# Performance work log

Hardware: AMD Instinct MI355X
Metric: run time of the kernel (lower is better)

Reference implementation:

```python
import jax, jax.numpy as jnp
import numpy as np

B, T, D, H = 2, 2048, 1024, 16
HS = D // H  # head_size = 64


def setup_inputs() -> dict:
    key = jax.random.key(0)
    ks = jax.random.split(key, 8)
    scale = D ** -0.5
    q = jax.random.normal(ks[0], (B, T, D), dtype=jnp.float32)
    k = jax.random.normal(ks[1], (B, T, D), dtype=jnp.float32)
    v = jax.random.normal(ks[2], (B, T, D), dtype=jnp.float32)
    # per-head projection weights (no bias), stacked over heads: [H, D, HS]
    Wq = jax.random.normal(ks[3], (H, D, HS), dtype=jnp.float32) * scale
    Wk = jax.random.normal(ks[4], (H, D, HS), dtype=jnp.float32) * scale
    Wv = jax.random.normal(ks[5], (H, D, HS), dtype=jnp.float32) * scale
    # output projection Linear(H*HS, D) with bias
    Wo = jax.random.normal(ks[6], (D, D), dtype=jnp.float32) * scale
    bo = jnp.zeros((D,), dtype=jnp.float32)
    # causal mask, broadcastable to [B, T, T]; mask==0 -> -inf
    mask = jnp.tril(jnp.ones((T, T), dtype=bool))[None]
    return {"q": q, "k": k, "v": v, "Wq": Wq, "Wk": Wk, "Wv": Wv,
            "Wo": Wo, "bo": bo, "mask": mask}


def reference(q, k, v, Wq, Wk, Wv, Wo, bo, mask):
    # Batched equivalent of the per-head loop: project all heads at once.
    Q = jnp.einsum('btc,hcd->bhtd', q, Wq)  # [B,H,T,HS]
    K = jnp.einsum('btc,hcd->bhtd', k, Wk)
    V = jnp.einsum('btc,hcd->bhtd', v, Wv)
    wei = jnp.einsum('bhtd,bhsd->bhts', Q, K) * (HS ** -0.5)  # [B,H,T,T]
    wei = jnp.where(mask[:, None, :, :], wei, jnp.float32(-jnp.inf))
    attn = jax.nn.softmax(wei, axis=-1)  # dropout is identity in eval
    out = jnp.einsum('bhts,bhsd->bhtd', attn, V)
    out = out.transpose(0, 2, 1, 3).reshape(B, T, D)  # concat heads
    return out @ Wo + bo
```

## Files before the change

### kernel.cpp

```cpp
#include <hip/hip_runtime.h>
#include <hip/hip_bf16.h>
#include <math.h>

#define BB 2
#define TT 2048
#define DM 1024
#define NH 16
#define HS 64
#define MM (BB*TT)

typedef __attribute__((ext_vector_type(8))) short s16x8;
typedef __attribute__((ext_vector_type(4))) float f32x4;

#define MFMA16(a,b,c) __builtin_amdgcn_mfma_f32_16x16x32_bf16((a),(b),(c),0,0,0)

__device__ inline unsigned short f2bf(float f) {
    union { float f; unsigned u; } x; x.f = f;
    unsigned r = x.u + 0x7fff + ((x.u >> 16) & 1);
    return (unsigned short)(r >> 16);
}
__device__ inline unsigned short f2bfr(float f) {
    union { float f; unsigned u; } x; x.f = f;
    return (unsigned short)((x.u + 0x8000u) >> 16);
}

__device__ __forceinline__ void gload16(const void* g, void* l) {
    __builtin_amdgcn_global_load_lds(
        (const __attribute__((address_space(1))) unsigned int*)g,
        (__attribute__((address_space(3))) unsigned int*)l, 16, 0, 0);
}

__global__ __launch_bounds__(256) void cvt_w_kernel(
    const float* __restrict__ W0, const float* __restrict__ W1,
    const float* __restrict__ W2, unsigned short* __restrict__ dst, int wo_mode)
{
    __shared__ __align__(16) short Tt[64 * 72];
    const int t = threadIdx.x;
    const int d0 = blockIdx.x * 64;
    const int h  = blockIdx.y;
    const int z  = blockIdx.z;
    const float* W = (z == 0) ? W0 : (z == 1) ? W1 : W2;
    unsigned short* dz = dst + (size_t)z * DM * DM;

    #pragma unroll
    for (int it = 0; it < 16; ++it) {
        int dl = it * 4 + (t >> 6);
        int hs = t & 63;
        float vv = wo_mode ? W[(size_t)(d0 + dl) * DM + h * 64 + hs]
                           : W[(size_t)h * DM * HS + (size_t)(d0 + dl) * HS + hs];
        Tt[hs * 72 + dl] = (short)f2bf(vv);
    }
    __syncthreads();
    int hs = t >> 2, doff = (t & 3) * 16;
    s16x8 r0 = *(s16x8*)&Tt[hs * 72 + doff];
    s16x8 r1 = *(s16x8*)&Tt[hs * 72 + doff + 8];
    unsigned short* op = dz + (size_t)(h * 64 + hs) * DM + d0 + doff;
    *(s16x8*)op = r0;
    *(s16x8*)(op + 8) = r1;
}

__global__ __launch_bounds__(256) void proj_gemm_kernel(
    const float* __restrict__ q, const float* __restrict__ k,
    const float* __restrict__ v, const unsigned short* __restrict__ Wt,
    unsigned short* __restrict__ Qb, unsigned short* __restrict__ Kb,
    unsigned short* __restrict__ Vt)
{
    __shared__ __align__(16) float As[2][128 * 32];
    __shared__ __align__(16) unsigned short Bs[2][128 * 32];

    const int tid = threadIdx.x;
    const int l = tid & 63, w = tid >> 6;
    const int wr = w >> 1, wc = w & 1;
    const int g = l >> 4, r16 = l & 15;

    const int bid = blockIdx.x;
    const int xcd = bid & 7, u = bid >> 3;
    const int z = u >> 5, vv = u & 31;
    const int n0 = (vv >> 2) * 128;
    const int m0 = (xcd * 4 + (vv & 3)) * 128;

    const float* x = (z == 0) ? q : (z == 1) ? k : v;
    const unsigned short* Wz = Wt + (size_t)z * DM * DM;

    const float* aS[4]; int aDof[4];
    #pragma unroll
    for (int p = 0; p < 4; ++p) {
        int qid = p * 256 + tid;
        int row = qid >> 3, gl = qid & 7;
        int col = ((gl ^ (row & 7)) * 4);
        aS[p] = x + (size_t)(m0 + row) * DM + col;
        aDof[p] = qid * 4;
    }
    const unsigned short* bS[2]; int bDof[2];
    #pragma unroll
    for (int p = 0; p < 2; ++p) {
        int qid = p * 256 + tid;
        int row = qid >> 2, gl = qid & 3;
        int col = ((gl ^ ((row >> 1) & 3)) * 8);
        bS[p] = Wz + (size_t)(n0 + row) * DM + col;
        bDof[p] = qid * 8;
    }

    int aoff[4][2], boff[4];
    #pragma unroll
    for (int i = 0; i < 4; ++i) {
        int row = wr * 64 + i * 16 + r16;
        int s = row & 7;
        aoff[i][0] = row * 32 + ((2 * g) ^ s) * 4;
        aoff[i][1] = row * 32 + ((2 * g + 1) ^ s) * 4;
    }
    #pragma unroll
    for (int c = 0; c < 4; ++c) {
        int row = wc * 64 + c * 16 + r16;
        boff[c] = row * 32 + (g ^ ((row >> 1) & 3)) * 8;
    }

    f32x4 acc[4][4];
    #pragma unroll
    for (int i = 0; i < 4; ++i)
        #pragma unroll
        for (int c = 0; c < 4; ++c)
            #pragma unroll
            for (int j = 0; j < 4; ++j) acc[i][c][j] = 0.0f;

    #define PSTAGE(buf, k0_) do {                                        \
        _Pragma("unroll")                                                \
        for (int p = 0; p < 4; ++p)                                      \
            gload16(aS[p] + (k0_), &As[(buf)][aDof[p]]);                 \
        _Pragma("unroll")                                                \
        for (int p = 0; p < 2; ++p)                                      \
            gload16(bS[p] + (k0_), &Bs[(buf)][bDof[p]]);                 \
    } while (0)

    #define PCOMPUTE(buf) do {                                           \
        s16x8 af[4], bf[4];                                              \
        _Pragma("unroll")                                                \
        for (int i = 0; i < 4; ++i) {                                    \
            float4 lo = *(const float4*)&As[(buf)][aoff[i][0]];          \
            float4 hi = *(const float4*)&As[(buf)][aoff[i][1]];          \
            union { s16x8 v; __hip_bfloat162 h[4]; } cv;                 \
            cv.h[0] = __float22bfloat162_rn(make_float2(lo.x, lo.y));    \
            cv.h[1] = __float22bfloat162_rn(make_float2(lo.z, lo.w));    \
            cv.h[2] = __float22bfloat162_rn(make_float2(hi.x, hi.y));    \
            cv.h[3] = __float22bfloat162_rn(make_float2(hi.z, hi.w));    \
            af[i] = cv.v;                                                \
        }                                                                \
        _Pragma("unroll")                                                \
        for (int c = 0; c < 4; ++c) bf[c] = *(const s16x8*)&Bs[(buf)][boff[c]]; \
        _Pragma("unroll")                                                \
        for (int i = 0; i < 4; ++i)                                      \
            _Pragma("unroll")                                            \
            for (int c = 0; c < 4; ++c)                                  \
                acc[i][c] = MFMA16(af[i], bf[c], acc[i][c]);             \
    } while (0)

    PSTAGE(0, 0);
    for (int t = 0; t < 31; ++t) {
        PSTAGE((t + 1) & 1, (t + 1) * 32);
        asm volatile("s_waitcnt vmcnt(6)" ::: "memory");
        __builtin_amdgcn_sched_barrier(0);
        __builtin_amdgcn_s_barrier();
        PCOMPUTE(t & 1);
        __builtin_amdgcn_s_barrier();
    }
    asm volatile("s_waitcnt vmcnt(0)" ::: "memory");
    __builtin_amdgcn_sched_barrier(0);
    __builtin_amdgcn_s_barrier();
    PCOMPUTE(1);
    #undef PSTAGE
    #undef PCOMPUTE

    const int h = (n0 >> 6) + wc;
    if (z != 2) {
        unsigned short* dst = (z == 0) ? Qb : Kb;
        const float sc = (z == 0) ? 0.18033688011112042f : 1.0f;
        #pragma unroll
        for (int i = 0; i < 4; ++i)
            #pragma unroll
            for (int j = 0; j < 4; ++j) {
                int row = m0 + wr * 64 + i * 16 + g * 4 + j;
                int bb = row >> 11, tt = row & (TT - 1);
                size_t rb = (((size_t)(bb * NH + h)) * TT + tt) * HS;
                #pragma unroll
                for (int c = 0; c < 4; ++c)
                    dst[rb + c * 16 + r16] = f2bf(acc[i][c][j] * sc);
            }
    } else {
        #pragma unroll
        for (int i = 0; i < 4; ++i) {
            int row0 = m0 + wr * 64 + i * 16 + g * 4;
            int bb = row0 >> 11, tt0 = row0 & (TT - 1);
            #pragma unroll
            for (int c = 0; c < 4; ++c) {
                int hs = c * 16 + r16;
                union { unsigned long long u; unsigned short s[4]; } pk;
                #pragma unroll
                for (int j = 0; j < 4; ++j) pk.s[j] = f2bf(acc[i][c][j]);
                *(unsigned long long*)&Vt[(((size_t)(bb * NH + h)) * HS + hs) * TT + tt0] = pk.u;
            }
        }
    }
}

__global__ __launch_bounds__(256) void out_gemm_kernel(
    const unsigned short* __restrict__ Ob, const unsigned short* __restrict__ Wot,
    const float* __restrict__ bo, float* __restrict__ out)
{
    __shared__ __align__(16) unsigned short As2[128 * 32];
    __shared__ __align__(16) unsigned short Bs2[128 * 32];

    const int tid = threadIdx.x;
    const int l = tid & 63, w = tid >> 6;
    const int wr = w >> 1, wc = w & 1;
    const int g = l >> 4, r16 = l & 15;
    const int m0 = blockIdx.y * 128;
    const int n0 = blockIdx.x * 128;

    const unsigned short* aS[2]; unsigned short* aD[2];
    const unsigned short* bS[2]; unsigned short* bD[2];
    #pragma unroll
    for (int p = 0; p < 2; ++p) {
        int qid = p * 256 + tid;
        int row = qid >> 2, gl = qid & 3;
        int col = ((gl ^ ((row >> 1) & 3)) * 8);
        aS[p] = Ob + (size_t)(m0 + row) * DM + col;
        aD[p] = As2 + qid * 8;
        bS[p] = Wot + (size_t)(n0 + row) * DM + col;
        bD[p] = Bs2 + qid * 8;
    }

    int aoff[4], boff[4];
    #pragma unroll
    for (int i = 0; i < 4; ++i) {
        int row = wr * 64 + i * 16 + r16;
        aoff[i] = row * 32 + (g ^ ((row >> 1) & 3)) * 8;
    }
    #pragma unroll
    for (int c = 0; c < 4; ++c) {
        int row = wc * 64 + c * 16 + r16;
        boff[c] = row * 32 + (g ^ ((row >> 1) & 3)) * 8;
    }

    f32x4 acc[4][4];
    #pragma unroll
    for (int i = 0; i < 4; ++i)
        #pragma unroll
        for (int c = 0; c < 4; ++c)
            #pragma unroll
            for (int j = 0; j < 4; ++j) acc[i][c][j] = 0.0f;

    for (int k0 = 0; k0 < DM; k0 += 32) {
        #pragma unroll
        for (int p = 0; p < 2; ++p) gload16(aS[p] + k0, aD[p]);
        #pragma unroll
        for (int p = 0; p < 2; ++p) gload16(bS[p] + k0, bD[p]);
        __syncthreads();

        s16x8 af[4], bf[4];
        #pragma unroll
        for (int i = 0; i < 4; ++i) af[i] = *(const s16x8*)&As2[aoff[i]];
        #pragma unroll
        for (int c = 0; c < 4; ++c) bf[c] = *(const s16x8*)&Bs2[boff[c]];
        #pragma unroll
        for (int i = 0; i < 4; ++i)
            #pragma unroll
            for (int c = 0; c < 4; ++c)
                acc[i][c] = MFMA16(af[i], bf[c], acc[i][c]);
        __syncthreads();
    }

    #pragma unroll
    for (int i = 0; i < 4; ++i)
        #pragma unroll
        for (int j = 0; j < 4; ++j) {
            int row = m0 + wr * 64 + i * 16 + g * 4 + j;
            #pragma unroll
            for (int c = 0; c < 4; ++c) {
                int col = n0 + wc * 64 + c * 16 + r16;
                out[(size_t)row * DM + col] = acc[i][c][j] + bo[col];
            }
        }
}

template<bool MASKED>
__device__ __forceinline__ void ftile6(
    int kv0, int t0, int r16, int g,
    const unsigned short* __restrict__ Kl,
    const unsigned short* __restrict__ Vl,
    short* __restrict__ Pw,
    const s16x8 (&qf)[2],
    float (&l_part)[4], f32x4 (&o)[4])
{
    const int rs = r16 & 7;
    float pe[4][4];
    #pragma unroll
    for (int c = 0; c < 4; ++c) {
        if (!MASKED || (kv0 + c * 16 <= t0 + 15)) {
            f32x4 s0;
            #pragma unroll
            for (int j = 0; j < 4; ++j) s0[j] = 0.0f;
            const int base = (c * 16 + r16) * 64;
            s16x8 kf0 = *(const s16x8*)&Kl[base + ((g ^ rs) * 8)];
            s16x8 kf1 = *(const s16x8*)&Kl[base + (((4 + g) ^ rs) * 8)];
            s0 = MFMA16(qf[0], kf0, s0);
            s0 = MFMA16(qf[1], kf1, s0);
            #pragma unroll
            for (int j = 0; j < 4; ++j) {
                float e = __builtin_amdgcn_exp2f(s0[j] - 16.0f);
                if (MASKED)
                    e = (kv0 + c * 16 + r16 <= t0 + g * 4 + j) ? e : 0.0f;
                pe[c][j] = e;
                l_part[j] += e;
            }
        } else {
            #pragma unroll
            for (int j = 0; j < 4; ++j) pe[c][j] = 0.0f;
        }
    }

    #pragma unroll
    for (int c = 0; c < 2; ++c)
        #pragma unroll
        for (int j = 0; j < 4; ++j)
            Pw[(g * 4 + j) * 36 + c * 16 + r16] = (short)f2bfr(pe[c][j]);
    s16x8 pa0 = *(const s16x8*)&Pw[r16 * 36 + g * 8];
    #pragma unroll
    for (int c = 0; c < 4; ++c) {
        s16x8 vf = *(const s16x8*)&Vl[(c * 16 + r16) * 64 + ((g ^ rs) * 8)];
        o[c] = MFMA16(pa0, vf, o[c]);
    }

    if (!MASKED || (kv0 + 32 <= t0 + 15)) {
        #pragma unroll
        for (int c = 0; c < 2; ++c)
            #pragma unroll
            for (int j = 0; j < 4; ++j)
                Pw[(g * 4 + j) * 36 + c * 16 + r16] = (short)f2bfr(pe[2 + c][j]);
        s16x8 pa1 = *(const s16x8*)&Pw[r16 * 36 + g * 8];
        #pragma unroll
        for (int c = 0; c < 4; ++c) {
            s16x8 vf = *(const s16x8*)&Vl[(c * 16 + r16) * 64 + (((4 + g) ^ rs) * 8)];
            o[c] = MFMA16(pa1, vf, o[c]);
        }
    }
}

__global__ __launch_bounds__(256) void flash6_kernel(
    const unsigned short* __restrict__ Qb,
    const unsigned short* __restrict__ Kb,
    const unsigned short* __restrict__ Vt,
    unsigned short* __restrict__ Ob)
{
    __shared__ __align__(16) unsigned short Kls[2][4096];
    __shared__ __align__(16) unsigned short Vls[2][4096];
    __shared__ __align__(16) short Pl[4][576];

    const int tid = threadIdx.x;
    const int l = tid & 63, w = tid >> 6;
    const int r16 = l & 15, g = l >> 4;

    const int bid = blockIdx.x;
    const int bh = bid & 31;
    const int jj = (bid >> 5) & 7;
    const int ii = bid >> 8;
    const int qc = ii * 8 + ((ii & 1) ? (7 - jj) : jj);
    const int numt = qc + 1;
    const int b = bh >> 4, h = bh & 15;

    const unsigned short* Qp = Qb + (size_t)bh * TT * HS;
    const unsigned short* Kp = Kb + (size_t)bh * TT * HS;
    const unsigned short* Vp = Vt + (size_t)bh * HS * TT;
    unsigned short* Op = Ob + (size_t)b * TT * DM + h * HS;
    short* Pw = Pl[w];

    const int t0 = qc * 64 + w * 16;

    const int srow0 = tid >> 3, c8 = tid & 7;
    const int srow1 = 32 + srow0;
    const unsigned short* kS0 = Kp + srow0 * HS + ((c8 ^ (srow0 & 7)) * 8);
    const unsigned short* kS1 = Kp + srow1 * HS + ((c8 ^ (srow1 & 7)) * 8);
    const unsigned short* vS0 = Vp + (size_t)srow0 * TT + ((c8 ^ (srow0 & 7)) * 8);
    const unsigned short* vS1 = Vp + (size_t)srow1 * TT + ((c8 ^ (srow1 & 7)) * 8);
    const int d0 = tid * 8, d1 = 2048 + tid * 8;

    s16x8 qf[2];
    #pragma unroll
    for (int s = 0; s < 2; ++s)
        qf[s] = *(const s16x8*)(Qp + (size_t)(t0 + r16) * HS + s * 32 + g * 8);

    float l_part[4] = {0.0f, 0.0f, 0.0f, 0.0f};
    f32x4 o[4];
    #pragma unroll
    for (int c = 0; c < 4; ++c)
        #pragma unroll
        for (int j = 0; j < 4; ++j) o[c][j] = 0.0f;

    #define STAGE(buf, kv0_) do {                                   \
        gload16(kS0 + (size_t)(kv0_) * HS, &Kls[(buf)][d0]);        \
        gload16(kS1 + (size_t)(kv0_) * HS, &Kls[(buf)][d1]);        \
        gload16(vS0 + (kv0_), &Vls[(buf)][d0]);                     \
        gload16(vS1 + (kv0_), &Vls[(buf)][d1]);                     \
    } while (0)

    STAGE(0, 0);
    for (int t = 0; t < numt - 1; ++t) {
        STAGE((t + 1) & 1, (t + 1) * 64);
        asm volatile("s_waitcnt vmcnt(4)" ::: "memory");
        __builtin_amdgcn_sched_barrier(0);
        __builtin_amdgcn_s_barrier();
        ftile6<false>(t * 64, t0, r16, g, &Kls[t & 1][0], &Vls[t & 1][0],
                      Pw, qf, l_part, o);
        __builtin_amdgcn_s_barrier();
    }
    asm volatile("s_waitcnt vmcnt(0)" ::: "memory");
    __builtin_amdgcn_sched_barrier(0);
    __builtin_amdgcn_s_barrier();
    ftile6<true>((numt - 1) * 64, t0, r16, g,
                 &Kls[(numt - 1) & 1][0], &Vls[(numt - 1) & 1][0],
                 Pw, qf, l_part, o);
    #undef STAGE

    #pragma unroll
    for (int j = 0; j < 4; ++j) {
        float ls = l_part[j];
        ls += __shfl_xor(ls, 1);
        ls += __shfl_xor(ls, 2);
        ls += __shfl_xor(ls, 4);
        ls += __shfl_xor(ls, 8);
        float inv = 1.0f / ls;
        int t = t0 + g * 4 + j;
        #pragma unroll
        for (int c = 0; c < 4; ++c)
            Op[(size_t)t * DM + c * 16 + r16] = f2bfr(o[c][j] * inv);
    }
}

extern "C" void kernel_launch(void* const* d_in, const int* in_sizes, int n_in,
                              void* d_out, int out_size, void* d_ws, size_t ws_size,
                              hipStream_t stream) {
    const float* q  = (const float*)d_in[0];
    const float* k  = (const float*)d_in[1];
    const float* v  = (const float*)d_in[2];
    const float* Wq = (const float*)d_in[3];
    const float* Wk = (const float*)d_in[4];
    const float* Wv = (const float*)d_in[5];
    const float* Wo = (const float*)d_in[6];
    const float* bo = (const float*)d_in[7];
    float* out = (float*)d_out;

    const size_t QKV_ELEMS = (size_t)BB * NH * TT * HS;
    unsigned short* Qb = (unsigned short*)d_ws;
    unsigned short* Kb = Qb + QKV_ELEMS;
    unsigned short* Vt = Kb + QKV_ELEMS;
    unsigned short* R4 = Vt + QKV_ELEMS;
    unsigned short* Wt = R4;
    unsigned short* Ob = R4;
    unsigned short* Wot = Qb;

    cvt_w_kernel<<<dim3(16, 16, 3), 256, 0, stream>>>(Wq, Wk, Wv, Wt, 0);
    proj_gemm_kernel<<<dim3(768), 256, 0, stream>>>(q, k, v, Wt, Qb, Kb, Vt);
    flash6_kernel<<<dim3(1024), 256, 0, stream>>>(Qb, Kb, Vt, Ob);
    cvt_w_kernel<<<dim3(16, 16, 1), 256, 0, stream>>>(Wo, Wo, Wo, Wot, 1);
    out_gemm_kernel<<<dim3(8, 32), 256, 0, stream>>>(Ob, Wot, bo, out);
}
```

Baseline: 133.6 us.

## Convert proj A tile to bf16 in registers, double-buffer out GEMM with XCD swizzle

The projection GEMM now loads fp32 activations into registers, converts them to bf16 once and stores bf16 into LDS. Previously each wave read fp32 from LDS and converted per MFMA operand, so this halves LDS footprint and read traffic and removes redundant conversions. The cost is that the A load is now a synchronous register load rather than a direct-to-LDS async load. The output GEMM gains double-buffered async LDS staging with vmcnt waits and an XCD-aware block remapping onto a 1D grid, aiming to overlap loads with MFMA and improve L2 locality.

```diff
diff --git a/kernel.cpp b/kernel.cpp
--- a/kernel.cpp
+++ b/kernel.cpp
@@ -65,7 +65,7 @@
     unsigned short* __restrict__ Qb, unsigned short* __restrict__ Kb,
     unsigned short* __restrict__ Vt)
 {
-    __shared__ __align__(16) float As[2][128 * 32];
+    __shared__ __align__(16) unsigned short As[2][128 * 32];
     __shared__ __align__(16) unsigned short Bs[2][128 * 32];
 
     const int tid = threadIdx.x;
@@ -82,15 +82,13 @@
     const float* x = (z == 0) ? q : (z == 1) ? k : v;
     const unsigned short* Wz = Wt + (size_t)z * DM * DM;
 
-    const float* aS[4]; int aDof[4];
-    #pragma unroll
-    for (int p = 0; p < 4; ++p) {
-        int qid = p * 256 + tid;
-        int row = qid >> 3, gl = qid & 7;
-        int col = ((gl ^ (row & 7)) * 4);
-        aS[p] = x + (size_t)(m0 + row) * DM + col;
-        aDof[p] = qid * 4;
-    }
+    const int ar = tid >> 1;
+    const int sA = (tid & 1) * 2;
+    const float* axp = x + (size_t)(m0 + ar) * DM + (tid & 1) * 16;
+    const int axr = (ar >> 1) & 3;
+    const int awof0 = ar * 32 + ((sA ^ axr) * 8);
+    const int awof1 = ar * 32 + (((sA + 1) ^ axr) * 8);
+
     const unsigned short* bS[2]; int bDof[2];
     #pragma unroll
     for (int p = 0; p < 2; ++p) {
@@ -101,18 +99,16 @@
         bDof[p] = qid * 8;
     }
 
-    int aoff[4][2], boff[4];
+    int aoff[4], boff[4];
     #pragma unroll
     for (int i = 0; i < 4; ++i) {
         int row = wr * 64 + i * 16 + r16;
-        int s = row & 7;
-        aoff[i][0] = row * 32 + ((2 * g) ^ s) * 4;
-        aoff[i][1] = row * 32 + ((2 * g + 1) ^ s) * 4;
+        aoff[i] = row * 32 + ((g ^ ((row >> 1) & 3)) * 8);
     }
     #pragma unroll
     for (int c = 0; c < 4; ++c) {
         int row = wc * 64 + c * 16 + r16;
-        boff[c] = row * 32 + (g ^ ((row >> 1) & 3)) * 8;
+        boff[c] = row * 32 + ((g ^ ((row >> 1) & 3)) * 8);
     }
 
     f32x4 acc[4][4];
@@ -123,28 +119,36 @@
             #pragma unroll
             for (int j = 0; j < 4; ++j) acc[i][c][j] = 0.0f;
 
-    #define PSTAGE(buf, k0_) do {                                        \
-        _Pragma("unroll")                                                \
-        for (int p = 0; p < 4; ++p)                                      \
-            gload16(aS[p] + (k0_), &As[(buf)][aDof[p]]);                 \
-        _Pragma("unroll")                                                \
-        for (int p = 0; p < 2; ++p)                                      \
-            gload16(bS[p] + (k0_), &Bs[(buf)][bDof[p]]);                 \
+    float4 al0, al1, al2, al3;
+
+    #define PLOAD(k0_) do {                                              \
+        const float* ap = axp + (k0_);                                   \
+        al0 = *(const float4*)(ap);                                      \
+        al1 = *(const float4*)(ap + 4);                                  \
+        al2 = *(const float4*)(ap + 8);                                  \
+        al3 = *(const float4*)(ap + 12);                                 \
+        gload16(bS[0] + (k0_), &Bs[bufn][bDof[0]]);                      \
+        gload16(bS[1] + (k0_), &Bs[bufn][bDof[1]]);                      \
+    } while (0)
+
+    #define PSTORE() do {                                                \
+        union { s16x8 v; __hip_bfloat162 h[4]; } c0, c1;                 \
+        c0.h[0] = __float22bfloat162_rn(make_float2(al0.x, al0.y));      \
+        c0.h[1] = __float22bfloat162_rn(make_float2(al0.z, al0.w));      \
+        c0.h[2] = __float22bfloat162_rn(make_float2(al1.x, al1.y));      \
+        c0.h[3] = __float22bfloat162_rn(make_float2(al1.z, al1.w));      \
+        c1.h[0] = __float22bfloat162_rn(make_float2(al2.x, al2.y));      \
+        c1.h[1] = __float22bfloat162_rn(make_float2(al2.z, al2.w));      \
+        c1.h[2] = __float22bfloat162_rn(make_float2(al3.x, al3.y));      \
+        c1.h[3] = __float22bfloat162_rn(make_float2(al3.z, al3.w));      \
+        *(s16x8*)&As[bufn][awof0] = c0.v;                                \
+        *(s16x8*)&As[bufn][awof1] = c1.v;                                \
     } while (0)
 
     #define PCOMPUTE(buf) do {                                           \
         s16x8 af[4], bf[4];                                              \
         _Pragma("unroll")                                                \
-        for (int i = 0; i < 4; ++i) {                                    \
-            float4 lo = *(const float4*)&As[(buf)][aoff[i][0]];          \
-            float4 hi = *(const float4*)&As[(buf)][aoff[i][1]];          \
-            union { s16x8 v; __hip_bfloat162 h[4]; } cv;                 \
-            cv.h[0] = __float22bfloat162_rn(make_float2(lo.x, lo.y));    \
-            cv.h[1] = __float22bfloat162_rn(make_float2(lo.z, lo.w));    \
-            cv.h[2] = __float22bfloat162_rn(make_float2(hi.x, hi.y));    \
-            cv.h[3] = __float22bfloat162_rn(make_float2(hi.z, hi.w));    \
-            af[i] = cv.v;                                                \
-        }                                                                \
+        for (int i = 0; i < 4; ++i) af[i] = *(const s16x8*)&As[(buf)][aoff[i]]; \
         _Pragma("unroll")                                                \
         for (int c = 0; c < 4; ++c) bf[c] = *(const s16x8*)&Bs[(buf)][boff[c]]; \
         _Pragma("unroll")                                                \
@@ -154,20 +158,22 @@
                 acc[i][c] = MFMA16(af[i], bf[c], acc[i][c]);             \
     } while (0)
 
-    PSTAGE(0, 0);
+    {
+        int bufn = 0;
+        PLOAD(0);
+        PSTORE();
+    }
+    __syncthreads();
     for (int t = 0; t < 31; ++t) {
-        PSTAGE((t + 1) & 1, (t + 1) * 32);
-        asm volatile("s_waitcnt vmcnt(6)" ::: "memory");
-        __builtin_amdgcn_sched_barrier(0);
-        __builtin_amdgcn_s_barrier();
-        PCOMPUTE(t & 1);
-        __builtin_amdgcn_s_barrier();
-    }
-    asm volatile("s_waitcnt vmcnt(0)" ::: "memory");
-    __builtin_amdgcn_sched_barrier(0);
-    __builtin_amdgcn_s_barrier();
+        const int cur = t & 1, bufn = cur ^ 1;
+        PLOAD((t + 1) * 32);
+        PCOMPUTE(cur);
+        PSTORE();
+        __syncthreads();
+    }
     PCOMPUTE(1);
-    #undef PSTAGE
+    #undef PLOAD
+    #undef PSTORE
     #undef PCOMPUTE
 
     const int h = (n0 >> 6) + wc;
@@ -206,39 +212,41 @@
     const unsigned short* __restrict__ Ob, const unsigned short* __restrict__ Wot,
     const float* __restrict__ bo, float* __restrict__ out)
 {
-    __shared__ __align__(16) unsigned short As2[128 * 32];
-    __shared__ __align__(16) unsigned short Bs2[128 * 32];
+    __shared__ __align__(16) unsigned short As2[2][128 * 32];
+    __shared__ __align__(16) unsigned short Bs2[2][128 * 32];
 
     const int tid = threadIdx.x;
     const int l = tid & 63, w = tid >> 6;
     const int wr = w >> 1, wc = w & 1;
     const int g = l >> 4, r16 = l & 15;
-    const int m0 = blockIdx.y * 128;
-    const int n0 = blockIdx.x * 128;
-
-    const unsigned short* aS[2]; unsigned short* aD[2];
-    const unsigned short* bS[2]; unsigned short* bD[2];
+
+    const int bid = blockIdx.x;
+    const int xcd = bid & 7, u = bid >> 3;
+    const int n0 = (u >> 2) * 128;
+    const int m0 = (xcd * 4 + (u & 3)) * 128;
+
+    const unsigned short* aS[2]; const unsigned short* bS[2];
+    int sDof[2];
     #pragma unroll
     for (int p = 0; p < 2; ++p) {
         int qid = p * 256 + tid;
         int row = qid >> 2, gl = qid & 3;
         int col = ((gl ^ ((row >> 1) & 3)) * 8);
         aS[p] = Ob + (size_t)(m0 + row) * DM + col;
-        aD[p] = As2 + qid * 8;
         bS[p] = Wot + (size_t)(n0 + row) * DM + col;
-        bD[p] = Bs2 + qid * 8;
+        sDof[p] = qid * 8;
     }
 
     int aoff[4], boff[4];
     #pragma unroll
     for (int i = 0; i < 4; ++i) {
         int row = wr * 64 + i * 16 + r16;
-        aoff[i] = row * 32 + (g ^ ((row >> 1) & 3)) * 8;
+        aoff[i] = row * 32 + ((g ^ ((row >> 1) & 3)) * 8);
     }
     #pragma unroll
     for (int c = 0; c < 4; ++c) {
         int row = wc * 64 + c * 16 + r16;
-        boff[c] = row * 32 + (g ^ ((row >> 1) & 3)) * 8;
+        boff[c] = row * 32 + ((g ^ ((row >> 1) & 3)) * 8);
     }
 
     f32x4 acc[4][4];
@@ -249,25 +257,42 @@
             #pragma unroll
             for (int j = 0; j < 4; ++j) acc[i][c][j] = 0.0f;
 
-    for (int k0 = 0; k0 < DM; k0 += 32) {
-        #pragma unroll
-        for (int p = 0; p < 2; ++p) gload16(aS[p] + k0, aD[p]);
-        #pragma unroll
-        for (int p = 0; p < 2; ++p) gload16(bS[p] + k0, bD[p]);
-        __syncthreads();
-
-        s16x8 af[4], bf[4];
-        #pragma unroll
-        for (int i = 0; i < 4; ++i) af[i] = *(const s16x8*)&As2[aoff[i]];
-        #pragma unroll
-        for (int c = 0; c < 4; ++c) bf[c] = *(const s16x8*)&Bs2[boff[c]];
-        #pragma unroll
-        for (int i = 0; i < 4; ++i)
-            #pragma unroll
-            for (int c = 0; c < 4; ++c)
-                acc[i][c] = MFMA16(af[i], bf[c], acc[i][c]);
-        __syncthreads();
-    }
+    #define OSTAGE(buf, k0_) do {                                        \
+        _Pragma("unroll")                                                \
+        for (int p = 0; p < 2; ++p) {                                    \
+            gload16(aS[p] + (k0_), &As2[(buf)][sDof[p]]);                \
+            gload16(bS[p] + (k0_), &Bs2[(buf)][sDof[p]]);                \
+        }                                                                \
+    } while (0)
+
+    #define OCOMPUTE(buf) do {                                           \
+        s16x8 af[4], bf[4];                                              \
+        _Pragma("unroll")                                                \
+        for (int i = 0; i < 4; ++i) af[i] = *(const s16x8*)&As2[(buf)][aoff[i]]; \
+        _Pragma("unroll")                                                \
+        for (int c = 0; c < 4; ++c) bf[c] = *(const s16x8*)&Bs2[(buf)][boff[c]]; \
+        _Pragma("unroll")                                                \
+        for (int i = 0; i < 4; ++i)                                      \
+            _Pragma("unroll")                                            \
+            for (int c = 0; c < 4; ++c)                                  \
+                acc[i][c] = MFMA16(af[i], bf[c], acc[i][c]);             \
+    } while (0)
+
+    OSTAGE(0, 0);
+    for (int t = 0; t < 31; ++t) {
+        OSTAGE((t + 1) & 1, (t + 1) * 32);
+        asm volatile("s_waitcnt vmcnt(4)" ::: "memory");
+        __builtin_amdgcn_sched_barrier(0);
+        __builtin_amdgcn_s_barrier();
+        OCOMPUTE(t & 1);
+        __builtin_amdgcn_s_barrier();
+    }
+    asm volatile("s_waitcnt vmcnt(0)" ::: "memory");
+    __builtin_amdgcn_sched_barrier(0);
+    __builtin_amdgcn_s_barrier();
+    OCOMPUTE(1);
+    #undef OSTAGE
+    #undef OCOMPUTE
 
     #pragma unroll
     for (int i = 0; i < 4; ++i)
@@ -461,5 +486,5 @@
     proj_gemm_kernel<<<dim3(768), 256, 0, stream>>>(q, k, v, Wt, Qb, Kb, Vt);
     flash6_kernel<<<dim3(1024), 256, 0, stream>>>(Qb, Kb, Vt, Ob);
     cvt_w_kernel<<<dim3(16, 16, 1), 256, 0, stream>>>(Wo, Wo, Wo, Wot, 1);
-    out_gemm_kernel<<<dim3(8, 32), 256, 0, stream>>>(Ob, Wot, bo, out);
-}
+    out_gemm_kernel<<<dim3(256), 256, 0, stream>>>(Ob, Wot, bo, out);
+}
```

After: 141.4 us. 5.8% more time.
